# Kernel tuning notes

Hardware: AMD Instinct MI355X
Metric: run time of the kernel (lower is better)

The kernel has to match this reference:

```python
import jax, jax.numpy as jnp
import numpy as np

MWH, MWW = 8, 32  # max_window_size from __init__
NUM_HEADS = 16
DIM = 512


def _relative_position_index(wh, ww):
    # static (wh, ww are python ints) -> [N, N] int index into bias table
    ch = np.arange(wh)
    cw = np.arange(ww)
    coords = np.stack(np.meshgrid(ch, cw, indexing='ij'))  # [2, wh, ww]
    cf = coords.reshape(2, -1)                              # [2, N]
    rel = cf[:, :, None] - cf[:, None, :]                   # [2, N, N]
    rel = rel.transpose(1, 2, 0).copy()                     # [N, N, 2]
    rel[:, :, 0] += MWH - 1
    rel[:, :, 1] += MWW - 1
    rel[:, :, 0] *= 2 * MWW - 1
    return jnp.asarray(rel.sum(-1))                         # [N, N]


def setup_inputs() -> dict:
    key = jax.random.key(0)
    ks = jax.random.split(key, 8)
    B_, N, C = 128, 256, DIM
    max_pos = (2 * MWH - 1) * (2 * MWW - 1)  # 945
    return {
        'x': jax.random.normal(ks[0], (B_, N, C), dtype=jnp.float32),
        'q_global': jax.random.normal(ks[1], (1, 1), dtype=jnp.float32),
        'qkv_w': jax.random.normal(ks[2], (3 * C, C), dtype=jnp.float32) * (1.0 / np.sqrt(C)),
        'qkv_b': jnp.zeros((3 * C,), dtype=jnp.float32),
        'proj_w': jax.random.normal(ks[3], (C, C), dtype=jnp.float32) * (1.0 / np.sqrt(C)),
        'proj_b': jnp.zeros((C,), dtype=jnp.float32),
        'rpb_table': jax.random.truncated_normal(ks[4], -2.0, 2.0, (max_pos, NUM_HEADS), dtype=jnp.float32) * 0.02,
        'wh': 8,
        'ww': 32,
    }


def reference(x, q_global, qkv_w, qkv_b, proj_w, proj_b, rpb_table, wh, ww):
    B_, N, C = x.shape
    H = NUM_HEADS
    hd = C // H
    scale = hd ** -0.5

    rpi = _relative_position_index(wh, ww)  # [N, N]

    qkv = x @ qkv_w.T + qkv_b                       # [B_, N, 3C]
    qkv = qkv.reshape(B_, N, 3, H, hd).transpose(2, 0, 3, 1, 4)  # [3, B_, H, N, hd]
    q, k, v = qkv[0], qkv[1], qkv[2]

    attn = jnp.einsum('bhnd,bhmd->bhnm', q * scale, k)  # [B_, H, N, N]
    bias = rpb_table[rpi.reshape(-1)].reshape(N, N, H).transpose(2, 0, 1)  # [H, N, N]
    attn = jax.nn.softmax(attn + bias[None], axis=-1)

    out = jnp.einsum('bhnm,bhmd->bhnd', attn, v)     # [B_, H, N, hd]
    out = out.transpose(0, 2, 1, 3).reshape(B_, N, C)
    return out @ proj_w.T + proj_b
```

## Files before the change

### kernel.cpp

```cpp
#include <hip/hip_runtime.h>
#include <hip/hip_fp16.h>
#include <cstdint>

typedef _Float16 f16x8 __attribute__((ext_vector_type(8)));
typedef _Float16 f16x4 __attribute__((ext_vector_type(4)));
typedef float    f32x4 __attribute__((ext_vector_type(4)));

#define MFMA16(a, b, c) __builtin_amdgcn_mfma_f32_16x16x32_f16((a), (b), (c), 0, 0, 0)

__device__ __forceinline__ void async16(_Float16* lds, const _Float16* g) {
    __builtin_amdgcn_global_load_lds(
        (const __attribute__((address_space(1))) void*)g,
        (__attribute__((address_space(3))) void*)lds, 16, 0, 0);
}

__global__ __launch_bounds__(256) void k_cvt(
    const float* __restrict__ src, _Float16* __restrict__ dst)
{
    const int i = blockIdx.x * 256 + threadIdx.x;
    const float4 a = ((const float4*)src)[2 * i];
    const float4 b = ((const float4*)src)[2 * i + 1];
    f16x8 o = { (_Float16)a.x, (_Float16)a.y, (_Float16)a.z, (_Float16)a.w,
                (_Float16)b.x, (_Float16)b.y, (_Float16)b.z, (_Float16)b.w };
    ((f16x8*)dst)[i] = o;
}

__global__ __launch_bounds__(256) void k_gemm_f16(
    const _Float16* __restrict__ A, int lda,
    const _Float16* __restrict__ B, int ldb,
    const float* __restrict__ bias,
    _Float16* __restrict__ C, int ldc,
    int K, int nTilesN, int cpx)
{
    __shared__ _Float16 lA[128 * 64];
    __shared__ _Float16 lB[128 * 64];
    const int t    = threadIdx.x;
    const int lane = t & 63, wv = t >> 6;
    const int fr = lane & 15, fg = lane >> 4;
    const int wrow = (wv >> 1) * 64, wcol = (wv & 1) * 64;

    const int gid  = (blockIdx.x & 7) * cpx + (blockIdx.x >> 3);
    const int row0 = (gid / nTilesN) * 128;
    const int col0 = (gid % nTilesN) * 128;

    const int rowLane = lane >> 3;
    const int colOff  = ((lane & 7) ^ rowLane) * 8;
    const int wvr = wv * 32;

    const _Float16* Ag = A + (size_t)(row0 + wvr + rowLane) * lda + colOff;
    const _Float16* Bg = B + (size_t)(col0 + wvr + rowLane) * ldb + colOff;
    _Float16* lAw = &lA[wvr * 64];
    _Float16* lBw = &lB[wvr * 64];

    f32x4 acc[4][4] = {};

    for (int k0 = 0; k0 < K; k0 += 64) {
#pragma unroll
        for (int i = 0; i < 4; ++i) {
            async16(lAw + i * 8 * 64, Ag + k0 + (size_t)i * 8 * lda);
            async16(lBw + i * 8 * 64, Bg + k0 + (size_t)i * 8 * ldb);
        }
        __syncthreads();
#pragma unroll
        for (int kk = 0; kk < 2; ++kk) {
            f16x8 af[4], bf[4];
#pragma unroll
            for (int mi = 0; mi < 4; ++mi) {
                const int ra = wrow + mi * 16 + fr;
                const int rb = wcol + mi * 16 + fr;
                const int ch = ((kk * 4 + fg) ^ (fr & 7)) * 8;
                af[mi] = *(const f16x8*)&lA[ra * 64 + ch];
                bf[mi] = *(const f16x8*)&lB[rb * 64 + ch];
            }
#pragma unroll
            for (int mi = 0; mi < 4; ++mi)
#pragma unroll
                for (int ni = 0; ni < 4; ++ni)
                    acc[mi][ni] = MFMA16(af[mi], bf[ni], acc[mi][ni]);
        }
        __syncthreads();
    }

#pragma unroll
    for (int ni = 0; ni < 4; ++ni) {
        const int col = col0 + wcol + ni * 16 + fr;
        const float bb = bias[col];
#pragma unroll
        for (int mi = 0; mi < 4; ++mi)
#pragma unroll
            for (int r = 0; r < 4; ++r) {
                const int row = row0 + wrow + mi * 16 + fg * 4 + r;
                C[(size_t)row * ldc + col] = (_Float16)(acc[mi][ni][r] + bb);
            }
    }
}

__global__ __launch_bounds__(256) void k_proj_gemm(
    const _Float16* __restrict__ A, int lda, const float* __restrict__ B,
    const float* __restrict__ bias, float* __restrict__ C,
    int M, int N, int K)
{
    __shared__ _Float16 lA[64 * 64];
    __shared__ _Float16 lB[64 * 64];
    const int t    = threadIdx.x;
    const int lane = t & 63, wv = t >> 6;
    const int wr = (wv >> 1) * 32, wc = (wv & 1) * 32;
    const int fr = lane & 15, fg = lane >> 4;
    const int srow = t >> 2;
    const int scol = (t & 3) * 16;

    const _Float16* Ag = A + (size_t)(blockIdx.x * 64 + srow) * lda + scol;
    const float*    Bg = B + (size_t)(blockIdx.y * 64 + srow) * K + scol;

    f32x4 acc[2][2] = {};

    for (int k0 = 0; k0 < K; k0 += 64) {
#pragma unroll
        for (int q = 0; q < 2; ++q) {
            f16x8 av = *(const f16x8*)(Ag + k0 + q * 8);
            int bo = ((scol + q * 8) * 2) ^ ((srow & 7) << 4);
            *(f16x8*)((char*)lA + srow * 128 + bo) = av;
        }
#pragma unroll
        for (int q = 0; q < 4; ++q) {
            float4 bv = *(const float4*)(Bg + k0 + q * 4);
            int bo = ((scol + q * 4) * 2) ^ ((srow & 7) << 4);
            f16x4 bh = { (_Float16)bv.x, (_Float16)bv.y, (_Float16)bv.z, (_Float16)bv.w };
            *(f16x4*)((char*)lB + srow * 128 + bo) = bh;
        }
        __syncthreads();
#pragma unroll
        for (int kc = 0; kc < 2; ++kc) {
            const int kb = kc * 64 + fg * 16;
            f16x8 a0, a1, b0, b1;
            { int r = wr + fr;      a0 = *(const f16x8*)((char*)lA + r * 128 + (kb ^ ((r & 7) << 4))); }
            { int r = wr + 16 + fr; a1 = *(const f16x8*)((char*)lA + r * 128 + (kb ^ ((r & 7) << 4))); }
            { int r = wc + fr;      b0 = *(const f16x8*)((char*)lB + r * 128 + (kb ^ ((r & 7) << 4))); }
            { int r = wc + 16 + fr; b1 = *(const f16x8*)((char*)lB + r * 128 + (kb ^ ((r & 7) << 4))); }
            acc[0][0] = MFMA16(a0, b0, acc[0][0]);
            acc[0][1] = MFMA16(a0, b1, acc[0][1]);
            acc[1][0] = MFMA16(a1, b0, acc[1][0]);
            acc[1][1] = MFMA16(a1, b1, acc[1][1]);
        }
        __syncthreads();
    }
#pragma unroll
    for (int mi = 0; mi < 2; ++mi)
#pragma unroll
        for (int ni = 0; ni < 2; ++ni) {
            const int col = blockIdx.y * 64 + wc + ni * 16 + fr;
            const float bb = bias[col];
#pragma unroll
            for (int r = 0; r < 4; ++r) {
                const int row = blockIdx.x * 64 + wr + mi * 16 + fg * 4 + r;
                C[(size_t)row * N + col] = acc[mi][ni][r] + bb;
            }
        }
}

#define ATT_SCALE 0.17677669529663687f

__global__ __launch_bounds__(256) void k_attn(
    _Float16* __restrict__ qkv, const float* __restrict__ rpb)
{
    __shared__ _Float16 lS[4][16 * 264];
    __shared__ _Float16 lVt[32 * 264];
    __shared__ float    lbias[945];

    const int bh = blockIdx.x;
    const int b = bh >> 4, h = bh & 15;
    const int t = threadIdx.x, wv = t >> 6, lane = t & 63;
    const int fr = lane & 15, fg = lane >> 4;

    _Float16* qkv_b0 = qkv + (size_t)b * 256 * 1536;

    for (int p = t; p < 945; p += 256) lbias[p] = rpb[p * 16 + h];

    {
        const _Float16* vrow = qkv_b0 + (size_t)t * 1536 + 1024 + h * 32;
        f16x8 v0 = *(const f16x8*)(vrow);
        f16x8 v1 = *(const f16x8*)(vrow + 8);
        f16x8 v2 = *(const f16x8*)(vrow + 16);
        f16x8 v3 = *(const f16x8*)(vrow + 24);
#pragma unroll
        for (int d = 0; d < 8; ++d) {
            lVt[(d     ) * 264 + t] = v0[d];
            lVt[(d +  8) * 264 + t] = v1[d];
            lVt[(d + 16) * 264 + t] = v2[d];
            lVt[(d + 24) * 264 + t] = v3[d];
        }
    }
    __syncthreads();

    _Float16* myS = &lS[wv][0];

    for (int rb = 0; rb < 4; ++rb) {
        const int r0 = wv * 64 + rb * 16;

        f16x8 aq = *(const f16x8*)(qkv_b0 + (size_t)(r0 + fr) * 1536 + h * 32 + fg * 8);

        float smax[4] = { -1e30f, -1e30f, -1e30f, -1e30f };
#pragma unroll 4
        for (int jt = 0; jt < 16; ++jt) {
            f16x8 bk = *(const f16x8*)(qkv_b0 + (size_t)(jt * 16 + fr) * 1536 + 512 + h * 32 + fg * 8);
            f32x4 s = { 0.f, 0.f, 0.f, 0.f };
            s = MFMA16(aq, bk, s);
            const int j  = jt * 16 + fr;
            const int jh = j >> 5, jw = j & 31;
#pragma unroll
            for (int r = 0; r < 4; ++r) {
                const int i  = r0 + fg * 4 + r;
                const int ih = i >> 5, iw = i & 31;
                float sv = s[r] * ATT_SCALE + lbias[(ih - jh + 7) * 63 + (iw - jw + 31)];
                smax[r] = fmaxf(smax[r], sv);
                myS[(fg * 4 + r) * 264 + j] = (_Float16)sv;
            }
        }
#pragma unroll
        for (int m = 1; m <= 8; m <<= 1)
#pragma unroll
            for (int r = 0; r < 4; ++r)
                smax[r] = fmaxf(smax[r], __shfl_xor(smax[r], m));
        float rmax;
        {
            float m0 = __shfl(smax[0], (fr >> 2) << 4);
            float m1 = __shfl(smax[1], (fr >> 2) << 4);
            float m2 = __shfl(smax[2], (fr >> 2) << 4);
            float m3 = __shfl(smax[3], (fr >> 2) << 4);
            float ma = (fr & 1) ? m1 : m0;
            float mb = (fr & 1) ? m3 : m2;
            rmax = (fr & 2) ? mb : ma;
        }
        asm volatile("s_waitcnt lgkmcnt(0)" ::: "memory");

        f16x8 pa[8];
        float rsum = 0.f;
#pragma unroll
        for (int kc = 0; kc < 8; ++kc) {
            f16x8 sv = *(const f16x8*)(&myS[fr * 264 + kc * 32 + fg * 8]);
            f16x8 ph;
#pragma unroll
            for (int jj = 0; jj < 8; ++jj) {
                float p = __expf((float)sv[jj] - rmax);
                rsum += p;
                ph[jj] = (_Float16)p;
            }
            pa[kc] = ph;
        }
        rsum += __shfl_xor(rsum, 16);
        rsum += __shfl_xor(rsum, 32);

        f32x4 o[2] = {};
#pragma unroll
        for (int kc = 0; kc < 8; ++kc) {
            f16x8 bv0 = *(const f16x8*)(&lVt[(fr     ) * 264 + kc * 32 + fg * 8]);
            f16x8 bv1 = *(const f16x8*)(&lVt[(fr + 16) * 264 + kc * 32 + fg * 8]);
            o[0] = MFMA16(pa[kc], bv0, o[0]);
            o[1] = MFMA16(pa[kc], bv1, o[1]);
        }
        float os[4];
#pragma unroll
        for (int r = 0; r < 4; ++r) os[r] = __shfl(rsum, fg * 4 + r);

#pragma unroll
        for (int ni = 0; ni < 2; ++ni)
#pragma unroll
            for (int r = 0; r < 4; ++r) {
                const int i = r0 + fg * 4 + r;
                const int d = ni * 16 + fr;
                qkv_b0[(size_t)i * 1536 + h * 32 + d] = (_Float16)(o[ni][r] / os[r]);
            }
    }
}

extern "C" void kernel_launch(void* const* d_in, const int* in_sizes, int n_in,
                              void* d_out, int out_size, void* d_ws, size_t ws_size,
                              hipStream_t stream)
{
    (void)in_sizes; (void)n_in;
    const float* x      = (const float*)d_in[0];
    const float* qkv_w  = (const float*)d_in[2];
    const float* qkv_b  = (const float*)d_in[3];
    const float* proj_w = (const float*)d_in[4];
    const float* proj_b = (const float*)d_in[5];
    const float* rpb    = (const float*)d_in[6];
    float* out = (float*)d_out;

    const int M  = 128 * 256;
    const int Cd = 512, N3 = 1536;

    const size_t need = (size_t)M * N3 * sizeof(_Float16);
    if (ws_size < need) {
        hipMemsetAsync(d_out, 0, (size_t)out_size * sizeof(float), stream);
        return;
    }

    _Float16* qkvh = (_Float16*)d_ws;
    _Float16* xh   = (_Float16*)d_out;
    _Float16* qwh  = xh + (size_t)M * Cd;

    k_cvt<<<dim3((M * Cd) / 2048), 256, 0, stream>>>(x, xh);
    k_cvt<<<dim3((N3 * Cd) / 2048), 256, 0, stream>>>(qkv_w, qwh);

    k_gemm_f16<<<dim3(3072), 256, 0, stream>>>(xh, Cd, qwh, Cd, qkv_b,
                                               qkvh, N3, Cd, 12, 384);
    k_attn<<<dim3(128 * 16), 256, 0, stream>>>(qkvh, rpb);
    k_proj_gemm<<<dim3(M / 64, Cd / 64), 256, 0, stream>>>(qkvh, N3, proj_w, proj_b, out, M, Cd, Cd);
}
```

Before: 365.7 us.

## Precompute dense fp16 bias matrix and retile projection GEMM to 128x128

Adds a kernel that expands the relative-position bias table into a dense per-head [256,256] fp16 matrix stored in the output buffer. The attention kernel then loads bias rows directly from it and computes the row max after adding the bias, replacing the per-element index math and the shuffle-based max reduction. The projection GEMM is replaced by a 128x128-tile kernel that loads A asynchronously into LDS and converts fp32 weights on the fly. Doing the bias addition in fp16 may slightly reduce precision, and the extra bias matrix costs a little more global memory traffic.

```diff
diff --git a/kernel.cpp b/kernel.cpp
--- a/kernel.cpp
+++ b/kernel.cpp
@@ -25,6 +25,15 @@
     ((f16x8*)dst)[i] = o;
 }
 
+__global__ __launch_bounds__(256) void k_bias(
+    const float* __restrict__ rpb, _Float16* __restrict__ bm)
+{
+    const int i = blockIdx.x & 255, j = threadIdx.x, h = blockIdx.x >> 8;
+    const int ih = i >> 5, iw = i & 31, jh = j >> 5, jw = j & 31;
+    const int idx = (ih - jh + 7) * 63 + (iw - jw + 31);
+    bm[(size_t)blockIdx.x * 256 + j] = (_Float16)rpb[idx * 16 + h];
+}
+
 __global__ __launch_bounds__(256) void k_gemm_f16(
     const _Float16* __restrict__ A, int lda,
     const _Float16* __restrict__ B, int ldb,
@@ -80,7 +89,6 @@
         }
         __syncthreads();
     }
-
 #pragma unroll
     for (int ni = 0; ni < 4; ++ni) {
         const int col = col0 + wcol + ni * 16 + fr;
@@ -95,77 +103,90 @@
     }
 }
 
-__global__ __launch_bounds__(256) void k_proj_gemm(
-    const _Float16* __restrict__ A, int lda, const float* __restrict__ B,
-    const float* __restrict__ bias, float* __restrict__ C,
-    int M, int N, int K)
-{
-    __shared__ _Float16 lA[64 * 64];
-    __shared__ _Float16 lB[64 * 64];
+__global__ __launch_bounds__(256) void k_gemm_pf32(
+    const _Float16* __restrict__ A, int lda,
+    const float* __restrict__ B, int ldb,
+    const float* __restrict__ bias,
+    float* __restrict__ C, int ldc,
+    int K, int nTilesN, int cpx)
+{
+    __shared__ _Float16 lA[128 * 64];
+    __shared__ _Float16 lB[128 * 64];
     const int t    = threadIdx.x;
     const int lane = t & 63, wv = t >> 6;
-    const int wr = (wv >> 1) * 32, wc = (wv & 1) * 32;
     const int fr = lane & 15, fg = lane >> 4;
-    const int srow = t >> 2;
-    const int scol = (t & 3) * 16;
-
-    const _Float16* Ag = A + (size_t)(blockIdx.x * 64 + srow) * lda + scol;
-    const float*    Bg = B + (size_t)(blockIdx.y * 64 + srow) * K + scol;
-
-    f32x4 acc[2][2] = {};
+    const int wrow = (wv >> 1) * 64, wcol = (wv & 1) * 64;
+
+    const int gid  = (blockIdx.x & 7) * cpx + (blockIdx.x >> 3);
+    const int row0 = (gid / nTilesN) * 128;
+    const int col0 = (gid % nTilesN) * 128;
+
+    const int rowLane = lane >> 3;
+    const int colOff  = ((lane & 7) ^ rowLane) * 8;
+    const int wvr = wv * 32;
+
+    const _Float16* Ag = A + (size_t)(row0 + wvr + rowLane) * lda + colOff;
+    _Float16* lAw = &lA[wvr * 64];
+
+    const int sb = t >> 1, cb = (t & 1) * 32;
+    const float* Bg = B + (size_t)(col0 + sb) * ldb + cb;
+
+    f32x4 acc[4][4] = {};
 
     for (int k0 = 0; k0 < K; k0 += 64) {
 #pragma unroll
-        for (int q = 0; q < 2; ++q) {
-            f16x8 av = *(const f16x8*)(Ag + k0 + q * 8);
-            int bo = ((scol + q * 8) * 2) ^ ((srow & 7) << 4);
-            *(f16x8*)((char*)lA + srow * 128 + bo) = av;
-        }
-#pragma unroll
-        for (int q = 0; q < 4; ++q) {
-            float4 bv = *(const float4*)(Bg + k0 + q * 4);
-            int bo = ((scol + q * 4) * 2) ^ ((srow & 7) << 4);
-            f16x4 bh = { (_Float16)bv.x, (_Float16)bv.y, (_Float16)bv.z, (_Float16)bv.w };
-            *(f16x4*)((char*)lB + srow * 128 + bo) = bh;
+        for (int i = 0; i < 4; ++i)
+            async16(lAw + i * 8 * 64, Ag + k0 + (size_t)i * 8 * lda);
+#pragma unroll
+        for (int c = 0; c < 4; ++c) {
+            float4 u = *(const float4*)(Bg + k0 + c * 8);
+            float4 v = *(const float4*)(Bg + k0 + c * 8 + 4);
+            f16x8 hv = { (_Float16)u.x, (_Float16)u.y, (_Float16)u.z, (_Float16)u.w,
+                         (_Float16)v.x, (_Float16)v.y, (_Float16)v.z, (_Float16)v.w };
+            const int ch = (cb >> 3) + c;
+            *(f16x8*)&lB[sb * 64 + ((ch ^ (sb & 7)) * 8)] = hv;
         }
         __syncthreads();
 #pragma unroll
-        for (int kc = 0; kc < 2; ++kc) {
-            const int kb = kc * 64 + fg * 16;
-            f16x8 a0, a1, b0, b1;
-            { int r = wr + fr;      a0 = *(const f16x8*)((char*)lA + r * 128 + (kb ^ ((r & 7) << 4))); }
-            { int r = wr + 16 + fr; a1 = *(const f16x8*)((char*)lA + r * 128 + (kb ^ ((r & 7) << 4))); }
-            { int r = wc + fr;      b0 = *(const f16x8*)((char*)lB + r * 128 + (kb ^ ((r & 7) << 4))); }
-            { int r = wc + 16 + fr; b1 = *(const f16x8*)((char*)lB + r * 128 + (kb ^ ((r & 7) << 4))); }
-            acc[0][0] = MFMA16(a0, b0, acc[0][0]);
-            acc[0][1] = MFMA16(a0, b1, acc[0][1]);
-            acc[1][0] = MFMA16(a1, b0, acc[1][0]);
-            acc[1][1] = MFMA16(a1, b1, acc[1][1]);
+        for (int kk = 0; kk < 2; ++kk) {
+            f16x8 af[4], bf[4];
+#pragma unroll
+            for (int mi = 0; mi < 4; ++mi) {
+                const int ra = wrow + mi * 16 + fr;
+                const int rb = wcol + mi * 16 + fr;
+                const int ch = ((kk * 4 + fg) ^ (fr & 7)) * 8;
+                af[mi] = *(const f16x8*)&lA[ra * 64 + ch];
+                bf[mi] = *(const f16x8*)&lB[rb * 64 + ch];
+            }
+#pragma unroll
+            for (int mi = 0; mi < 4; ++mi)
+#pragma unroll
+                for (int ni = 0; ni < 4; ++ni)
+                    acc[mi][ni] = MFMA16(af[mi], bf[ni], acc[mi][ni]);
         }
         __syncthreads();
     }
 #pragma unroll
-    for (int mi = 0; mi < 2; ++mi)
-#pragma unroll
-        for (int ni = 0; ni < 2; ++ni) {
-            const int col = blockIdx.y * 64 + wc + ni * 16 + fr;
-            const float bb = bias[col];
+    for (int ni = 0; ni < 4; ++ni) {
+        const int col = col0 + wcol + ni * 16 + fr;
+        const float bb = bias[col];
+#pragma unroll
+        for (int mi = 0; mi < 4; ++mi)
 #pragma unroll
             for (int r = 0; r < 4; ++r) {
-                const int row = blockIdx.x * 64 + wr + mi * 16 + fg * 4 + r;
-                C[(size_t)row * N + col] = acc[mi][ni][r] + bb;
-            }
-        }
+                const int row = row0 + wrow + mi * 16 + fg * 4 + r;
+                C[(size_t)row * ldc + col] = acc[mi][ni][r] + bb;
+            }
+    }
 }
 
 #define ATT_SCALE 0.17677669529663687f
 
 __global__ __launch_bounds__(256) void k_attn(
-    _Float16* __restrict__ qkv, const float* __restrict__ rpb)
+    _Float16* __restrict__ qkv, const _Float16* __restrict__ bm)
 {
     __shared__ _Float16 lS[4][16 * 264];
     __shared__ _Float16 lVt[32 * 264];
-    __shared__ float    lbias[945];
 
     const int bh = blockIdx.x;
     const int b = bh >> 4, h = bh & 15;
@@ -173,8 +194,7 @@
     const int fr = lane & 15, fg = lane >> 4;
 
     _Float16* qkv_b0 = qkv + (size_t)b * 256 * 1536;
-
-    for (int p = t; p < 945; p += 256) lbias[p] = rpb[p * 16 + h];
+    const _Float16* bias_h = bm + (size_t)h * 256 * 256;
 
     {
         const _Float16* vrow = qkv_b0 + (size_t)t * 1536 + 1024 + h * 32;
@@ -199,53 +219,46 @@
 
         f16x8 aq = *(const f16x8*)(qkv_b0 + (size_t)(r0 + fr) * 1536 + h * 32 + fg * 8);
 
-        float smax[4] = { -1e30f, -1e30f, -1e30f, -1e30f };
 #pragma unroll 4
         for (int jt = 0; jt < 16; ++jt) {
             f16x8 bk = *(const f16x8*)(qkv_b0 + (size_t)(jt * 16 + fr) * 1536 + 512 + h * 32 + fg * 8);
             f32x4 s = { 0.f, 0.f, 0.f, 0.f };
             s = MFMA16(aq, bk, s);
-            const int j  = jt * 16 + fr;
-            const int jh = j >> 5, jw = j & 31;
-#pragma unroll
-            for (int r = 0; r < 4; ++r) {
-                const int i  = r0 + fg * 4 + r;
-                const int ih = i >> 5, iw = i & 31;
-                float sv = s[r] * ATT_SCALE + lbias[(ih - jh + 7) * 63 + (iw - jw + 31)];
-                smax[r] = fmaxf(smax[r], sv);
-                myS[(fg * 4 + r) * 264 + j] = (_Float16)sv;
-            }
-        }
-#pragma unroll
-        for (int m = 1; m <= 8; m <<= 1)
 #pragma unroll
             for (int r = 0; r < 4; ++r)
-                smax[r] = fmaxf(smax[r], __shfl_xor(smax[r], m));
-        float rmax;
+                myS[(fg * 4 + r) * 264 + jt * 16 + fr] = (_Float16)(s[r] * ATT_SCALE);
+        }
+
+        f16x8 tb[8];
         {
-            float m0 = __shfl(smax[0], (fr >> 2) << 4);
-            float m1 = __shfl(smax[1], (fr >> 2) << 4);
-            float m2 = __shfl(smax[2], (fr >> 2) << 4);
-            float m3 = __shfl(smax[3], (fr >> 2) << 4);
-            float ma = (fr & 1) ? m1 : m0;
-            float mb = (fr & 1) ? m3 : m2;
-            rmax = (fr & 2) ? mb : ma;
+            const _Float16* brow = bias_h + (size_t)(r0 + fr) * 256 + fg * 8;
+#pragma unroll
+            for (int kc = 0; kc < 8; ++kc)
+                tb[kc] = *(const f16x8*)(brow + kc * 32);
         }
         asm volatile("s_waitcnt lgkmcnt(0)" ::: "memory");
 
-        f16x8 pa[8];
-        float rsum = 0.f;
+        float vmax = -1e30f;
 #pragma unroll
         for (int kc = 0; kc < 8; ++kc) {
             f16x8 sv = *(const f16x8*)(&myS[fr * 264 + kc * 32 + fg * 8]);
-            f16x8 ph;
-#pragma unroll
-            for (int jj = 0; jj < 8; ++jj) {
-                float p = __expf((float)sv[jj] - rmax);
+            tb[kc] = tb[kc] + sv;
+#pragma unroll
+            for (int j = 0; j < 8; ++j)
+                vmax = fmaxf(vmax, (float)tb[kc][j]);
+        }
+        vmax = fmaxf(vmax, __shfl_xor(vmax, 16));
+        vmax = fmaxf(vmax, __shfl_xor(vmax, 32));
+
+        float rsum = 0.f;
+#pragma unroll
+        for (int kc = 0; kc < 8; ++kc) {
+#pragma unroll
+            for (int j = 0; j < 8; ++j) {
+                float p = __expf((float)tb[kc][j] - vmax);
                 rsum += p;
-                ph[jj] = (_Float16)p;
-            }
-            pa[kc] = ph;
+                tb[kc][j] = (_Float16)p;
+            }
         }
         rsum += __shfl_xor(rsum, 16);
         rsum += __shfl_xor(rsum, 32);
@@ -255,8 +268,8 @@
         for (int kc = 0; kc < 8; ++kc) {
             f16x8 bv0 = *(const f16x8*)(&lVt[(fr     ) * 264 + kc * 32 + fg * 8]);
             f16x8 bv1 = *(const f16x8*)(&lVt[(fr + 16) * 264 + kc * 32 + fg * 8]);
-            o[0] = MFMA16(pa[kc], bv0, o[0]);
-            o[1] = MFMA16(pa[kc], bv1, o[1]);
+            o[0] = MFMA16(tb[kc], bv0, o[0]);
+            o[1] = MFMA16(tb[kc], bv1, o[1]);
         }
         float os[4];
 #pragma unroll
@@ -291,19 +304,22 @@
 
     const size_t need = (size_t)M * N3 * sizeof(_Float16);
     if (ws_size < need) {
-        hipMemsetAsync(d_out, 0, (size_t)out_size * sizeof(float), stream);
+        (void)hipMemsetAsync(d_out, 0, (size_t)out_size * sizeof(float), stream);
         return;
     }
 
     _Float16* qkvh = (_Float16*)d_ws;
     _Float16* xh   = (_Float16*)d_out;
     _Float16* qwh  = xh + (size_t)M * Cd;
+    _Float16* bmat = qwh + (size_t)N3 * Cd;
 
     k_cvt<<<dim3((M * Cd) / 2048), 256, 0, stream>>>(x, xh);
     k_cvt<<<dim3((N3 * Cd) / 2048), 256, 0, stream>>>(qkv_w, qwh);
+    k_bias<<<dim3(16 * 256), 256, 0, stream>>>(rpb, bmat);
 
     k_gemm_f16<<<dim3(3072), 256, 0, stream>>>(xh, Cd, qwh, Cd, qkv_b,
                                                qkvh, N3, Cd, 12, 384);
-    k_attn<<<dim3(128 * 16), 256, 0, stream>>>(qkvh, rpb);
-    k_proj_gemm<<<dim3(M / 64, Cd / 64), 256, 0, stream>>>(qkvh, N3, proj_w, proj_b, out, M, Cd, Cd);
-}
+    k_attn<<<dim3(128 * 16), 256, 0, stream>>>(qkvh, bmat);
+    k_gemm_pf32<<<dim3(1024), 256, 0, stream>>>(qkvh, N3, proj_w, Cd, proj_b,
+                                                out, Cd, Cd, 4, 128);
+}
```

New measurement: 371.0 us. About the same (+1.4%).
